# Performance work log

Hardware: AMD Instinct MI355X
Metric: run time of the kernel (lower is better)

The kernel has to match this reference:

```python
import jax, jax.numpy as jnp
import numpy as np
from functools import partial

K_NEIGHBORS = 9
GRID = 28            # hard-coded in AnomalyMapGenerator
OUT_HW = (224, 224)  # input_size
SIGMA = 4
RADIUS = int(4.0 * SIGMA + 0.5)  # scipy gaussian_filter truncate=4 -> 16


def avg_pool3(x):
    # torch.nn.AvgPool2d(3, 1, 1), count_include_pad=True -> window sum / 9
    s = jax.lax.reduce_window(x, 0.0, jax.lax.add, (1, 1, 3, 3), (1, 1, 1, 1),
                              [(0, 0), (0, 0), (1, 1), (1, 1)])
    return s / 9.0


def gaussian_filter2d(img):
    # scipy.ndimage.gaussian_filter, sigma=4, mode='reflect' (== numpy 'symmetric')
    xs = jnp.arange(-RADIUS, RADIUS + 1, dtype=img.dtype)
    k = jnp.exp(-(xs ** 2) / (2.0 * SIGMA * SIGMA))
    k = k / k.sum()
    conv = lambda v: jnp.convolve(v, k, mode='valid')
    p = jnp.pad(img, ((RADIUS, RADIUS), (0, 0)), mode='symmetric')
    img = jax.vmap(conv, in_axes=1, out_axes=1)(p)
    p = jnp.pad(img, ((0, 0), (RADIUS, RADIUS)), mode='symmetric')
    img = jax.vmap(conv, in_axes=0, out_axes=0)(p)
    return img


def setup_inputs() -> dict:
    key = jax.random.key(0)
    k1, k2, k3 = jax.random.split(key, 3)
    return {
        'features_layer2': jax.random.normal(k1, (1, 512, 28, 28), jnp.float32),
        'features_layer3': jax.random.normal(k2, (1, 1024, 14, 14), jnp.float32),
        'memory_bank': jax.random.normal(k3, (100000, 1536), jnp.float32),
    }


def reference(features_layer2, features_layer3, memory_bank):
    # 1) feature pooling (AvgPool2d(3,1,1)) per layer
    f2 = avg_pool3(features_layer2)   # [1, 512, 28, 28]
    f3 = avg_pool3(features_layer3)   # [1, 1024, 14, 14]

    # 2) concat_layer_embedding: unfold/fold == nearest-neighbor upsample + channel concat
    s = f2.shape[2] // f3.shape[2]    # stride = 2
    f3_up = jnp.repeat(jnp.repeat(f3, s, axis=2), s, axis=3)   # [1,1024,28,28]
    embedding = jnp.concatenate([f2, f3_up], axis=1)           # [1,1536,28,28]

    # 3) reshape_embedding: [B,E,H,W] -> [B*H*W, E]
    E = embedding.shape[1]
    emb = embedding.transpose(0, 2, 3, 1).reshape(-1, E)       # [784, 1536]

    # 4) brute-force kNN (euclidean) against memory bank, k=9
    d2 = (jnp.sum(emb * emb, axis=1, keepdims=True)
          + jnp.sum(memory_bank * memory_bank, axis=1)[None, :]
          - 2.0 * emb @ memory_bank.T)                         # [784, N]
    neg_top, _ = jax.lax.top_k(-d2, K_NEIGHBORS)               # smallest distances
    patch_scores = jnp.sqrt(jnp.clip(-neg_top, 1e-12))         # [784, 9]

    # 5) anomaly map: reshape 28x28 -> bilinear resize -> gaussian blur
    amap = patch_scores[:, 0].reshape(GRID, GRID)
    amap = jax.image.resize(amap, OUT_HW, method='bilinear')
    anomaly_map = gaussian_filter2d(amap)

    # 6) image-level anomaly score
    col0 = patch_scores[:, 0]
    conf = patch_scores[jnp.argmax(col0)]                      # [9]
    e = jnp.exp(conf)
    weight = 1.0 - jnp.max(e) / jnp.sum(e)
    anomaly_score = weight * jnp.max(col0)

    return anomaly_map, anomaly_score
```

## Files before the change

kernel.cpp:

```cpp
#include <hip/hip_runtime.h>

#define INFV 1e30f

typedef __attribute__((ext_vector_type(8))) short bf16x8;
typedef __attribute__((ext_vector_type(16))) float f32x16;

__device__ __forceinline__ unsigned short f2bf(float f){
  union { float f; unsigned u; } v; v.f = f;
  unsigned r = v.u + 0x7FFFu + ((v.u >> 16) & 1u);
  return (unsigned short)(r >> 16);
}
__device__ __forceinline__ float bf2f(unsigned short b){
  union { unsigned u; float f; } v; v.u = ((unsigned)b) << 16;
  return v.f;
}
__device__ __forceinline__ void async_cp16(void* lds, const void* g){
  __builtin_amdgcn_global_load_lds((const __attribute__((address_space(1))) unsigned int*)g,
                                   (__attribute__((address_space(3))) unsigned int*)lds,
                                   16, 0, 0);
}

__global__ void k_pool(const float* __restrict__ f2, const float* __restrict__ f3,
                       float* __restrict__ pf2, float* __restrict__ pf3){
  const int idx = blockIdx.x*256 + threadIdx.x;
  if (idx < 512*784){
    const int c = idx / 784, rem = idx % 784, y = rem / 28, x = rem % 28;
    const float* base = f2 + c*784;
    float s = 0.f;
    for (int dy = -1; dy <= 1; ++dy){
      int yy = y + dy; if (yy < 0 || yy > 27) continue;
      for (int dx = -1; dx <= 1; ++dx){
        int xx = x + dx; if (xx < 0 || xx > 27) continue;
        s += base[yy*28 + xx];
      }
    }
    pf2[idx] = s * (1.0f/9.0f);
  } else {
    const int j = idx - 512*784;
    if (j < 1024*196){
      const int c = j / 196, rem = j % 196, y = rem / 14, x = rem % 14;
      const float* base = f3 + c*196;
      float s = 0.f;
      for (int dy = -1; dy <= 1; ++dy){
        int yy = y + dy; if (yy < 0 || yy > 13) continue;
        for (int dx = -1; dx <= 1; ++dx){
          int xx = x + dx; if (xx < 0 || xx > 13) continue;
          s += base[yy*14 + xx];
        }
      }
      pf3[j] = s * (1.0f/9.0f);
    }
  }
}

__global__ void k_emb(const float* __restrict__ pf2, const float* __restrict__ pf3,
                      unsigned short* __restrict__ Aw, float* __restrict__ en2){
  __shared__ float red[256];
  const int p = blockIdx.x;
  const int t = threadIdx.x;
  const int y = p / 28, x = p % 28;
  float a2 = 0.f;
  for (int it = 0; it < 6; ++it){
    const int k = it*256 + t;
    float v = 0.f;
    if (p < 784){
      if (k < 512) v = pf2[k*784 + y*28 + x];
      else         v = pf3[(k - 512)*196 + (y >> 1)*14 + (x >> 1)];
    }
    a2 += v*v;
    const int chunk = k >> 5, kq = (k >> 3) & 3, j = k & 7;
    Aw[(size_t)chunk*26624 + (size_t)(kq*832 + p)*8 + j] = f2bf(v);
  }
  red[t] = a2;
  __syncthreads();
  for (int s = 128; s > 0; s >>= 1){
    if (t < s) red[t] += red[t + s];
    __syncthreads();
  }
  if (t == 0) en2[p] = red[0];
}

__global__ __launch_bounds__(768, 3) void k_gemm(const float* __restrict__ bank,
                                                 const unsigned short* __restrict__ Aw,
                                                 const float* __restrict__ en2,
                                                 float* __restrict__ pmin){
  __shared__ short As[26624];
  __shared__ short Bs[2048];
  __shared__ float en2s[832];
  __shared__ float bn2p[512];
  __shared__ float bn2v[64];

  const int tid = threadIdx.x;
  const int w = tid >> 6;
  const int lane = tid & 63;
  const int hi = lane >> 5;
  const int ln = lane & 31;
  const int n0 = blockIdx.x * 64;
  const int rm = (w < 2) ? 3 : 2;

  for (int i = tid; i < 832; i += 768) en2s[i] = en2[i];

  f32x16 acc[3][2];
  #pragma unroll
  for (int i = 0; i < 3; ++i)
    #pragma unroll
    for (int j = 0; j < 2; ++j)
      #pragma unroll
      for (int g = 0; g < 16; ++g) acc[i][j][g] = 0.0f;

  const int brow = tid >> 3;
  const int bpart = tid & 7;
  const bool bth = (tid < 512);
  const bool bvalid = bth && (n0 + brow < 100000);
  const float* bp = bank + (size_t)(n0 + brow) * 1536 + bpart * 4;
  const int bslot = ((bpart >> 1) * 64 + brow) * 8 + (bpart & 1) * 4;
  float s2 = 0.0f;

  const int row0 = w*64 + ln;
  const int row2 = 768 + w*32 + ln;

  for (int r = 0; r < 48; ++r){
    const unsigned short* Ag = Aw + (size_t)r * 26624;
    #pragma unroll
    for (int it = 0; it < 5; ++it){
      int u = it*768 + tid;
      if (u < 3328) async_cp16(&As[u*8], Ag + (size_t)u*8);
    }
    if (bth){
      float4 bv = make_float4(0.f, 0.f, 0.f, 0.f);
      if (bvalid) bv = *(const float4*)(bp + r*32);
      s2 += bv.x*bv.x + bv.y*bv.y + bv.z*bv.z + bv.w*bv.w;
      short4 sv;
      sv.x = (short)f2bf(bv.x); sv.y = (short)f2bf(bv.y);
      sv.z = (short)f2bf(bv.z); sv.w = (short)f2bf(bv.w);
      *(short4*)&Bs[bslot] = sv;
    }
    __syncthreads();
    #pragma unroll
    for (int s = 0; s < 2; ++s){
      const int kq = s*2 + hi;
      bf16x8 b0 = *(const bf16x8*)&Bs[(kq*64 + ln)*8];
      bf16x8 b1 = *(const bf16x8*)&Bs[(kq*64 + 32 + ln)*8];
      #pragma unroll
      for (int i = 0; i < 3; ++i){
        if (i < rm){
          const int rr = (i < 2) ? (row0 + i*32) : row2;
          bf16x8 a = *(const bf16x8*)&As[(kq*832 + rr)*8];
          acc[i][0] = __builtin_amdgcn_mfma_f32_32x32x16_bf16(a, b0, acc[i][0], 0, 0, 0);
          acc[i][1] = __builtin_amdgcn_mfma_f32_32x32x16_bf16(a, b1, acc[i][1], 0, 0, 0);
        }
      }
    }
    __syncthreads();
  }

  if (bth) bn2p[tid] = s2;
  __syncthreads();
  if (tid < 64){
    float t0 = 0.f;
    #pragma unroll
    for (int j = 0; j < 8; ++j) t0 += bn2p[tid*8 + j];
    bn2v[tid] = (n0 + tid < 100000) ? t0 : INFV;
  }
  __syncthreads();

  #pragma unroll
  for (int i = 0; i < 3; ++i){
    if (i < rm){
      const int mb = (i < 2) ? (w*64 + i*32) : (768 + w*32);
      float vv[16];
      #pragma unroll
      for (int g = 0; g < 16; ++g){
        const int m = mb + (g & 3) + 8*(g >> 2) + 4*hi;
        const float e2 = en2s[m];
        float d0 = e2 + bn2v[ln]      - 2.0f*acc[i][0][g];
        float d1 = e2 + bn2v[32 + ln] - 2.0f*acc[i][1][g];
        float v = fminf(d0, d1);
        #pragma unroll
        for (int off = 1; off < 32; off <<= 1)
          v = fminf(v, __shfl_xor(v, off, 64));
        vv[g] = v;
      }
      if (ln == 0){
        #pragma unroll
        for (int g = 0; g < 16; ++g){
          const int m = mb + (g & 3) + 8*(g >> 2) + 4*hi;
          pmin[(size_t)blockIdx.x * 832 + m] = vv[g];
        }
      }
    }
  }
}

__global__ void k_colmin(const float* __restrict__ pmin, float* __restrict__ col0){
  __shared__ float red[256];
  const int t = threadIdx.x;
  const int m0 = blockIdx.x * 64;
  const int m = m0 + (t & 63);
  const int g = t >> 6;
  float v = INFV;
  for (int b = g; b < 1563; b += 4) v = fminf(v, pmin[(size_t)b*832 + m]);
  red[t] = v;
  __syncthreads();
  if (t < 64){
    float vv = fminf(fminf(red[t], red[64+t]), fminf(red[128+t], red[192+t]));
    col0[m0 + t] = sqrtf(fmaxf(vv, 1e-12f));
  }
}

__global__ void k_argmax(const float* __restrict__ col0,
                         const float* __restrict__ pmin,
                         float* __restrict__ scal){
  __shared__ float red[256];
  __shared__ int redi[256];
  __shared__ float cand[1563];
  const int t = threadIdx.x;

  float best = -INFV; int bi = 0x7FFFFFFF;
  for (int m = t; m < 784; m += 256){
    float v = col0[m];
    if (v > best){ best = v; bi = m; }
  }
  red[t] = best; redi[t] = bi;
  __syncthreads();
  for (int s = 128; s > 0; s >>= 1){
    if (t < s){
      if (red[t+s] > red[t] || (red[t+s] == red[t] && redi[t+s] < redi[t])){
        red[t] = red[t+s]; redi[t] = redi[t+s];
      }
    }
    __syncthreads();
  }
  const int r = redi[0];
  const float maxv = red[0];
  __syncthreads();

  for (int b = t; b < 1563; b += 256) cand[b] = pmin[(size_t)b*832 + r];
  __syncthreads();

  float b9 = 0.f;
  for (int it = 0; it < 9; ++it){
    float lb = INFV; int li = -1;
    for (int b = t; b < 1563; b += 256){
      float v = cand[b];
      if (v < lb){ lb = v; li = b; }
    }
    red[t] = lb; redi[t] = li;
    __syncthreads();
    for (int s = 128; s > 0; s >>= 1){
      if (t < s && red[t+s] < red[t]){ red[t] = red[t+s]; redi[t] = redi[t+s]; }
      __syncthreads();
    }
    b9 = red[0];
    if (t == 0 && redi[0] >= 0) cand[redi[0]] = INFV;
    __syncthreads();
  }
  if (t == 0){
    ((int*)scal)[0] = r;
    scal[1] = maxv;
    scal[2] = b9 + 1.0f;
  }
}

__global__ void k_cand(const float* __restrict__ bank,
                       const unsigned short* __restrict__ Aw,
                       const float* __restrict__ en2,
                       const float* __restrict__ pmin,
                       const float* __restrict__ scal,
                       float* __restrict__ d2row){
  const int bid = blockIdx.x;
  const int t = threadIdx.x;
  const int r = ((const int*)scal)[0];
  const float thr = scal[2];
  const int n0 = bid * 64;

  if (pmin[(size_t)bid*832 + r] > thr){
    if (t < 64) d2row[n0 + t] = INFV;
    return;
  }
  __shared__ short er[1536];
  for (int k = t; k < 1536; k += 256){
    const int chunk = k >> 5, kq = (k >> 3) & 3, j = k & 7;
    er[k] = Aw[(size_t)chunk*26624 + (size_t)(kq*832 + r)*8 + j];
  }
  __syncthreads();
  const float e2r = en2[r];
  const int wv = t >> 6, ln = t & 63;
  for (int i = 0; i < 16; ++i){
    const int nl = wv*16 + i;
    const int n = n0 + nl;
    float dot = 0.f, b2 = 0.f;
    if (n < 100000){
      const float* bp2 = bank + (size_t)n * 1536;
      for (int k = ln; k < 1536; k += 64){
        float b = bp2[k];
        b2 += b*b;
        dot += bf2f(er[k]) * bf2f(f2bf(b));
      }
    }
    #pragma unroll
    for (int off = 1; off < 64; off <<= 1){
      dot += __shfl_xor(dot, off, 64);
      b2  += __shfl_xor(b2,  off, 64);
    }
    if (ln == 0) d2row[n] = (n < 100000) ? (e2r + b2 - 2.0f*dot) : INFV;
  }
}

__global__ void k_score(const float* __restrict__ d2row,
                        const float* __restrict__ scal,
                        float* __restrict__ outs){
  __shared__ float cs[2304];
  __shared__ float red[256];
  __shared__ int redi[256];
  __shared__ float nine[9];
  const int t = threadIdx.x;
  float loc[9];
  #pragma unroll
  for (int q = 0; q < 9; ++q) loc[q] = INFV;
  for (int n = t; n < 100000; n += 256){
    float v = d2row[n];
    if (v < loc[8]){
      loc[8] = v;
      #pragma unroll
      for (int q = 8; q > 0; --q){
        float a = fminf(loc[q-1], loc[q]);
        float b = fmaxf(loc[q-1], loc[q]);
        loc[q-1] = a; loc[q] = b;
      }
    }
  }
  #pragma unroll
  for (int q = 0; q < 9; ++q) cs[t*9 + q] = loc[q];
  __syncthreads();
  for (int it = 0; it < 9; ++it){
    float lb = INFV; int li = -1;
    for (int jx = t; jx < 2304; jx += 256){
      float v = cs[jx];
      if (v < lb){ lb = v; li = jx; }
    }
    red[t] = lb; redi[t] = li;
    __syncthreads();
    for (int s = 128; s > 0; s >>= 1){
      if (t < s && red[t+s] < red[t]){ red[t] = red[t+s]; redi[t] = redi[t+s]; }
      __syncthreads();
    }
    if (t == 0){ nine[it] = red[0]; if (redi[0] >= 0) cs[redi[0]] = INFV; }
    __syncthreads();
  }
  if (t == 0){
    float s[9];
    #pragma unroll
    for (int q = 0; q < 9; ++q) s[q] = sqrtf(fmaxf(nine[q], 1e-12f));
    const float mx = s[8];
    float sum = 0.f;
    #pragma unroll
    for (int q = 0; q < 9; ++q) sum += expf(s[q] - mx);
    const float weight = 1.0f - 1.0f/sum;
    outs[0] = weight * scal[1];
  }
}

__global__ void k_vblur(const float* __restrict__ col0, float* __restrict__ vmap){
  __shared__ float am[784];
  __shared__ float kw[33];
  const int t = threadIdx.x;
  for (int q = t; q < 784; q += 256) am[q] = col0[q];
  if (t < 33){ float d = (float)t - 16.0f; kw[t] = expf(-d*d*(1.0f/32.0f)); }
  __syncthreads();
  if (t == 0){
    float ss = 0.f;
    for (int q = 0; q < 33; ++q) ss += kw[q];
    const float inv = 1.0f/ss;
    for (int q = 0; q < 33; ++q) kw[q] *= inv;
  }
  __syncthreads();
  const int id = blockIdx.x*256 + t;
  const int i = id / 224, j = id % 224;
  const float ux = (j + 0.5f)*0.125f - 0.5f;
  const float fx0 = floorf(ux);
  const float fx = ux - fx0;
  int x0 = (int)fx0; int x1 = x0 + 1;
  x0 = max(0, min(27, x0)); x1 = max(0, min(27, x1));
  float a = 0.f;
  for (int d = 0; d < 33; ++d){
    int ii = i + d - 16;
    ii = (ii < 0) ? (-1 - ii) : ((ii > 223) ? (447 - ii) : ii);
    const float uy = (ii + 0.5f)*0.125f - 0.5f;
    const float fy0 = floorf(uy);
    const float fy = uy - fy0;
    int y0 = (int)fy0; int y1 = y0 + 1;
    y0 = max(0, min(27, y0)); y1 = max(0, min(27, y1));
    const float top = (1.0f - fx)*am[y0*28 + x0] + fx*am[y0*28 + x1];
    const float bot = (1.0f - fx)*am[y1*28 + x0] + fx*am[y1*28 + x1];
    a += kw[d]*((1.0f - fy)*top + fy*bot);
  }
  vmap[id] = a;
}

__global__ void k_hblur(const float* __restrict__ vmap, float* __restrict__ outm){
  __shared__ float rowb[256];
  __shared__ float kw[33];
  const int i = blockIdx.x;
  const int t = threadIdx.x;
  if (t < 33){ float d = (float)t - 16.0f; kw[t] = expf(-d*d*(1.0f/32.0f)); }
  __syncthreads();
  if (t == 0){
    float ss = 0.f;
    for (int q = 0; q < 33; ++q) ss += kw[q];
    const float inv = 1.0f/ss;
    for (int q = 0; q < 33; ++q) kw[q] *= inv;
  }
  int c = t - 16;
  c = (c < 0) ? (-1 - c) : ((c > 223) ? (447 - c) : c);
  rowb[t] = vmap[i*224 + c];
  __syncthreads();
  if (t < 224){
    float a = 0.f;
    #pragma unroll
    for (int d = 0; d < 33; ++d) a += kw[d]*rowb[t + d];
    outm[i*224 + t] = a;
  }
}

extern "C" void kernel_launch(void* const* d_in, const int* in_sizes, int n_in,
                              void* d_out, int out_size, void* d_ws, size_t ws_size,
                              hipStream_t stream) {
  const float* f2   = (const float*)d_in[0];
  const float* f3   = (const float*)d_in[1];
  const float* bank = (const float*)d_in[2];
  float* out = (float*)d_out;

  char* ws = (char*)d_ws;
  size_t off = 0;
  auto alloc = [&](size_t bytes) -> void* {
    void* p = ws + off;
    off += (bytes + 255) & ~(size_t)255;
    return p;
  };
  float* pf2           = (float*)alloc((size_t)512*784*4);
  float* pf3           = (float*)alloc((size_t)1024*196*4);
  unsigned short* A_ws = (unsigned short*)alloc((size_t)48*26624*2);
  float* en2           = (float*)alloc(832*4);
  float* pmin          = (float*)alloc((size_t)1563*832*4);
  float* col0          = (float*)alloc(832*4);
  float* scal          = (float*)alloc(64);
  float* d2row         = (float*)alloc(100032*4);
  float* vmap          = (float*)alloc((size_t)50176*4);

  k_pool  <<<2352, 256, 0, stream>>>(f2, f3, pf2, pf3);
  k_emb   <<<832,  256, 0, stream>>>(pf2, pf3, A_ws, en2);
  k_gemm  <<<1563, 768, 0, stream>>>(bank, A_ws, en2, pmin);
  k_colmin<<<13,   256, 0, stream>>>(pmin, col0);
  k_argmax<<<1,    256, 0, stream>>>(col0, pmin, scal);
  k_cand  <<<1563, 256, 0, stream>>>(bank, A_ws, en2, pmin, scal, d2row);
  k_score <<<1,    256, 0, stream>>>(d2row, scal, out + 50176);
  k_vblur <<<196,  256, 0, stream>>>(col0, vmap);
  k_hblur <<<224,  256, 0, stream>>>(vmap, out);
}
```

Before: 1.598 ms.

## Double-buffer A and B tiles in the kNN GEMM with async prefetch

The distance GEMM main loop now keeps two LDS buffers for the bf16 embedding tile and the memory-bank tile. The next K-chunk is loaded asynchronously into the spare buffer while MFMAs run on the current one, and the bank is staged as fp32 in LDS before conversion to bf16. The goal is to hide global-load latency inside each block instead of stalling at the barrier before compute. The catch is LDS use: per block it grows from about 62KB to about 136KB, which likely cuts resident blocks per CU from two to one, so the cross-block latency hiding this replaces may be lost.

```diff
diff --git a/kernel.cpp b/kernel.cpp
--- a/kernel.cpp
+++ b/kernel.cpp
@@ -84,8 +84,9 @@
                                                  const unsigned short* __restrict__ Aw,
                                                  const float* __restrict__ en2,
                                                  float* __restrict__ pmin){
-  __shared__ short As[26624];
-  __shared__ short Bs[2048];
+  __shared__ short As[2][26624];
+  __shared__ short Bs[2][2048];
+  __shared__ float Bf[2][2048];
   __shared__ float en2s[832];
   __shared__ float bn2p[512];
   __shared__ float bn2v[64];
@@ -119,39 +120,68 @@
   const int row0 = w*64 + ln;
   const int row2 = 768 + w*32 + ln;
 
-  for (int r = 0; r < 48; ++r){
-    const unsigned short* Ag = Aw + (size_t)r * 26624;
+  if (bvalid) async_cp16(&Bf[0][tid*4], bp);
+  {
+    const unsigned short* Ag = Aw;
     #pragma unroll
     for (int it = 0; it < 5; ++it){
       int u = it*768 + tid;
-      if (u < 3328) async_cp16(&As[u*8], Ag + (size_t)u*8);
-    }
-    if (bth){
+      if (u < 3328) async_cp16(&As[0][u*8], Ag + (size_t)u*8);
+    }
+  }
+  __syncthreads();
+  if (bth){
+    float4 bv = make_float4(0.f, 0.f, 0.f, 0.f);
+    if (bvalid) bv = *(const float4*)&Bf[0][tid*4];
+    s2 += bv.x*bv.x + bv.y*bv.y + bv.z*bv.z + bv.w*bv.w;
+    short4 sv;
+    sv.x = (short)f2bf(bv.x); sv.y = (short)f2bf(bv.y);
+    sv.z = (short)f2bf(bv.z); sv.w = (short)f2bf(bv.w);
+    *(short4*)&Bs[0][bslot] = sv;
+  }
+  __syncthreads();
+
+  int cur = 0;
+  for (int r = 0; r < 48; ++r){
+    const int nxt = cur ^ 1;
+    if (r < 47){
+      if (bvalid) async_cp16(&Bf[nxt][tid*4], bp + (r+1)*32);
+      const unsigned short* Ag = Aw + (size_t)(r+1) * 26624;
+      #pragma unroll
+      for (int it = 0; it < 5; ++it){
+        int u = it*768 + tid;
+        if (u < 3328) async_cp16(&As[nxt][u*8], Ag + (size_t)u*8);
+      }
+    }
+    const short* Ac = As[cur];
+    const short* Bc = Bs[cur];
+    #pragma unroll
+    for (int s = 0; s < 2; ++s){
+      const int kq = s*2 + hi;
+      bf16x8 b0 = *(const bf16x8*)&Bc[(kq*64 + ln)*8];
+      bf16x8 b1 = *(const bf16x8*)&Bc[(kq*64 + 32 + ln)*8];
+      #pragma unroll
+      for (int i = 0; i < 3; ++i){
+        if (i < rm){
+          const int rr = (i < 2) ? (row0 + i*32) : row2;
+          bf16x8 a = *(const bf16x8*)&Ac[(kq*832 + rr)*8];
+          acc[i][0] = __builtin_amdgcn_mfma_f32_32x32x16_bf16(a, b0, acc[i][0], 0, 0, 0);
+          acc[i][1] = __builtin_amdgcn_mfma_f32_32x32x16_bf16(a, b1, acc[i][1], 0, 0, 0);
+        }
+      }
+    }
+    __syncthreads();
+    if (r < 47 && bth){
       float4 bv = make_float4(0.f, 0.f, 0.f, 0.f);
-      if (bvalid) bv = *(const float4*)(bp + r*32);
+      if (bvalid) bv = *(const float4*)&Bf[nxt][tid*4];
       s2 += bv.x*bv.x + bv.y*bv.y + bv.z*bv.z + bv.w*bv.w;
       short4 sv;
       sv.x = (short)f2bf(bv.x); sv.y = (short)f2bf(bv.y);
       sv.z = (short)f2bf(bv.z); sv.w = (short)f2bf(bv.w);
-      *(short4*)&Bs[bslot] = sv;
-    }
-    __syncthreads();
-    #pragma unroll
-    for (int s = 0; s < 2; ++s){
-      const int kq = s*2 + hi;
-      bf16x8 b0 = *(const bf16x8*)&Bs[(kq*64 + ln)*8];
-      bf16x8 b1 = *(const bf16x8*)&Bs[(kq*64 + 32 + ln)*8];
-      #pragma unroll
-      for (int i = 0; i < 3; ++i){
-        if (i < rm){
-          const int rr = (i < 2) ? (row0 + i*32) : row2;
-          bf16x8 a = *(const bf16x8*)&As[(kq*832 + rr)*8];
-          acc[i][0] = __builtin_amdgcn_mfma_f32_32x32x16_bf16(a, b0, acc[i][0], 0, 0, 0);
-          acc[i][1] = __builtin_amdgcn_mfma_f32_32x32x16_bf16(a, b1, acc[i][1], 0, 0, 0);
-        }
-      }
-    }
-    __syncthreads();
+      *(short4*)&Bs[nxt][bslot] = sv;
+    }
+    __syncthreads();
+    cur = nxt;
   }
 
   if (bth) bn2p[tid] = s2;
```

Measured after the change: 1.598 ms. About the same (-0.0%).
